# Optimization experiments

Hardware: AMD Instinct MI355X
Metric: run time of the kernel (lower is better)

## Reference

```python
import jax, jax.numpy as jnp
import numpy as np

# Similarity layer (simnets-tf), L2 similarity, ksize=3x3, stride 1, SAME padding,
# no normalization term, out_of_bounds_value = 0.
# sim[b,n,i,j] = -sum_{c,p,q} |w[n,c,p,q]| * (x_patch[b,c,i+p,j+q] - t[n,c,p,q])^2
# Expanded: -conv(x^2, |w|) + 2*conv(x, |w|*t) - sum(|w|*t^2)  (exact since pad value is 0).

B, C, H, W = 16, 64, 112, 112
N, KH, KW = 256, 3, 3
PAD = 1  # SAME padding for ksize 3


def _conv(inp, ker):
    # inp: [B,C,H',W'] padded, ker: [N,C,KH,KW] -> [B,N,H,W], VALID
    return jax.lax.conv_general_dilated(
        inp, ker, window_strides=(1, 1), padding='VALID',
        dimension_numbers=('NCHW', 'OIHW', 'NCHW'))


def setup_inputs() -> dict:
    key = jax.random.key(0)
    k1, k2, k3 = jax.random.split(key, 3)
    x = jax.random.normal(k1, (B, C, H, W), dtype=jnp.float32)
    sweights = jax.random.normal(k2, (N, C, KH, KW), dtype=jnp.float32)
    templates = jax.random.normal(k3, (N, C, KH, KW), dtype=jnp.float32)
    return {'x': x, 'sweights': sweights, 'templates': templates}


def reference(x, sweights, templates):
    w = jnp.abs(sweights)                      # layer applies tf.abs to weights
    xp = jnp.pad(x, ((0, 0), (0, 0), (PAD, PAD), (PAD, PAD)),
                 constant_values=0.0)          # out_of_bounds_value = 0
    sq_term = _conv(xp * xp, w)                # sum w * x^2 -> [B,N,H,W]
    cross = _conv(xp, w * templates)           # sum w * t * x
    const = jnp.sum(w * templates * templates, axis=(1, 2, 3))  # [N]
    return -sq_term + 2.0 * cross - const[None, :, None, None]
```

## Files before the change

### kernel.cpp

```cpp
#include <hip/hip_runtime.h>
#include <stdint.h>

#define B_ 16
#define C_ 64
#define H_ 112
#define W_ 112
#define N_ 256

typedef __attribute__((ext_vector_type(8))) short short8;
typedef __attribute__((ext_vector_type(4))) float floatx4;

typedef __attribute__((address_space(1))) const uint32_t gas_u32;
typedef __attribute__((address_space(3))) uint32_t las_u32;

__device__ __forceinline__ uint32_t f2bf_bits(float f) {
  uint32_t u = __float_as_uint(f);
  return (u + 0x7fffu + ((u >> 16) & 1u)) >> 16;
}

__global__ __launch_bounds__(256) void xform_x(const float* __restrict__ x,
                                               uint32_t* __restrict__ xq) {
  __shared__ float ls[64][113];
  int bi = blockIdx.x;
  int b = bi / H_, i = bi % H_;
  const float* xbase = x + ((size_t)b * C_) * (H_ * W_) + (size_t)i * W_;
  for (int idx = threadIdx.x; idx < C_ * W_; idx += 256) {
    int c = idx / W_, j = idx - c * W_;
    ls[c][j] = xbase[(size_t)c * (H_ * W_) + j];
  }
  __syncthreads();
  uint32_t* orow = xq + ((size_t)(b * H_ + i)) * (W_ * C_);
  for (int idx = threadIdx.x; idx < W_ * C_; idx += 256) {
    int j = idx >> 6, c = idx & 63;
    float v = ls[c][j];
    float v2 = v * v;
    orow[idx] = f2bf_bits(v) | (f2bf_bits(v2) << 16);
  }
}

__global__ __launch_bounds__(64) void prep_wc(const float* __restrict__ sw,
                                              const float* __restrict__ tp,
                                              uint32_t* __restrict__ Wg,
                                              float* __restrict__ cN) {
  int n = blockIdx.x, c = threadIdx.x;
  int cg = c >> 5, ci = c & 31;
  int kk = ci >> 4, pos = ci & 15;
  const float* swp = sw + (size_t)(n * C_ + c) * 9;
  const float* tpp = tp + (size_t)(n * C_ + c) * 9;
  float s = 0.f;
#pragma unroll
  for (int tap = 0; tap < 9; ++tap) {
    float w = fabsf(swp[tap]);
    float t = tpp[tap];
    s += w * t * t;
    uint32_t v = f2bf_bits(2.0f * w * t) | (f2bf_bits(-w) << 16);
    Wg[(size_t)(((cg * 9 + tap) * 2 + kk) * (N_ * 16)) + n * 16 + pos] = v;
  }
#pragma unroll
  for (int off = 32; off > 0; off >>= 1) s += __shfl_down(s, off);
  if (c == 0) cN[n] = s;
}

__global__ __launch_bounds__(512, 4) void sim_main(const uint32_t* __restrict__ xq,
                                                   const uint32_t* __restrict__ Wg,
                                                   const float* __restrict__ cN,
                                                   float* __restrict__ out) {
  __shared__ uint32_t xs[18 * 18 * 32];
  __shared__ uint32_t ws[2 * 2048];

  int bx = blockIdx.x;
  int nb = bx & 1;
  bx >>= 1;
  int b = bx / 49;
  int rem = bx - b * 49;
  int rt = rem / 7, ct = rem - rt * 7;
  int r0 = rt * 16, c0 = ct * 16;
  int tid = threadIdx.x;
  int lane = tid & 63, wv = tid >> 6;
  int wn = wv & 1, wp = wv >> 1;
  int l15 = lane & 15, l4 = lane >> 4;

  floatx4 acc[4][4];
#pragma unroll
  for (int a = 0; a < 4; ++a)
#pragma unroll
    for (int p = 0; p < 4; ++p) acc[a][p] = (floatx4){0.f, 0.f, 0.f, 0.f};

  const uint32_t* xim = xq + (size_t)b * (H_ * W_ * C_);
  const uint32_t* wslice = Wg + nb * 2048;

  auto stage_xs = [&](int cg) {
    for (int idx = tid; idx < 324 * 8; idx += 512) {
      int s = idx >> 3, ch = idx & 7;
      int row = s / 18, col = s - row * 18;
      int gi = r0 - 1 + row, gj = c0 - 1 + col;
      uint4 v = make_uint4(0u, 0u, 0u, 0u);
      if ((unsigned)gi < (unsigned)H_ && (unsigned)gj < (unsigned)W_)
        v = *(const uint4*)(xim + ((size_t)(gi * W_ + gj)) * C_ + cg * 32 + ch * 4);
      *(uint4*)(&xs[s * 32 + ((ch ^ (s & 7)) << 2)]) = v;
    }
  };
  auto stage_w = [&](int step) {
    const uint32_t* g = wslice + (size_t)step * (N_ * 16) + wv * 256 + lane * 4;
    uint32_t* l = &ws[(step & 1) * 2048 + wv * 256];
    __builtin_amdgcn_global_load_lds((gas_u32*)g, (las_u32*)l, 16, 0, 0);
  };

  stage_xs(0);
  stage_w(0);
  __syncthreads();

  int awb = (wn * 64 + l15) * 16 + l4 * 4;

#pragma unroll 1
  for (int s = 0; s < 36; ++s) {
    if (s < 35) stage_w(s + 1);
    if (s == 18) {
      stage_xs(1);
      __syncthreads();
    }
    int t2 = (s < 18) ? s : s - 18;
    int tap = t2 >> 1, kk = t2 & 1;
    int dp = tap / 3, dq = tap - dp * 3;
    int chb = kk * 4 + l4;
    int buf = s & 1;

    short8 af[4], bfr[4];
#pragma unroll
    for (int nt = 0; nt < 4; ++nt)
      af[nt] = *(const short8*)(&ws[buf * 2048 + awb + nt * 256]);
#pragma unroll
    for (int pt = 0; pt < 4; ++pt) {
      int st = (wp * 4 + pt + dp) * 18 + l15 + dq;
      bfr[pt] = *(const short8*)(&xs[st * 32 + ((chb ^ (st & 7)) << 2)]);
    }
#pragma unroll
    for (int nt = 0; nt < 4; ++nt)
#pragma unroll
      for (int pt = 0; pt < 4; ++pt)
        acc[nt][pt] =
            __builtin_amdgcn_mfma_f32_16x16x32_bf16(af[nt], bfr[pt], acc[nt][pt], 0, 0, 0);
    if (s < 35) __syncthreads();
  }

#pragma unroll
  for (int nt = 0; nt < 4; ++nt) {
#pragma unroll
    for (int v = 0; v < 4; ++v) {
      int n = nb * 128 + wn * 64 + nt * 16 + l4 * 4 + v;
      float cv = cN[n];
#pragma unroll
      for (int pt = 0; pt < 4; ++pt) {
        int r = r0 + wp * 4 + pt;
        int col = c0 + l15;
        out[(((size_t)b * N_ + n) * H_ + r) * W_ + col] = acc[nt][pt][v] - cv;
      }
    }
  }
}

extern "C" void kernel_launch(void* const* d_in, const int* in_sizes, int n_in,
                              void* d_out, int out_size, void* d_ws, size_t ws_size,
                              hipStream_t stream) {
  const float* x = (const float*)d_in[0];
  const float* sw = (const float*)d_in[1];
  const float* tp = (const float*)d_in[2];
  float* out = (float*)d_out;

  const size_t xq_bytes = (size_t)B_ * H_ * W_ * C_ * 4;
  const size_t wg_bytes = (size_t)2 * 9 * 2 * N_ * 16 * 4;
  uint32_t* xq = (uint32_t*)d_ws;
  uint32_t* Wg = (uint32_t*)((char*)d_ws + xq_bytes);
  float* cN = (float*)((char*)d_ws + xq_bytes + wg_bytes);

  xform_x<<<dim3(B_ * H_), dim3(256), 0, stream>>>(x, xq);
  prep_wc<<<dim3(N_), dim3(64), 0, stream>>>(sw, tp, Wg, cN);
  sim_main<<<dim3(2 * B_ * 7 * 7), dim3(512), 0, stream>>>(xq, Wg, cN, out);
}
```

Before: 380.9 us.

## Deepen weight prefetch to four buffers and restage input in 16-channel chunks

Weight tiles are now prefetched two steps ahead into a four-slot LDS ring. The full __syncthreads per step is replaced with an explicit vmcnt wait followed by s_barrier, so one global->LDS load can stay in flight. The input tile is staged in four 16-channel chunks using a padded row stride of 20 words instead of the XOR swizzle, and the weight global layout is reordered to match the new fragment addressing. The aim is to hide weight-load latency behind MFMA work, at the cost of more frequent input restaging and its extra barriers.

```diff
diff --git a/kernel.cpp b/kernel.cpp
--- a/kernel.cpp
+++ b/kernel.cpp
@@ -43,10 +43,10 @@
                                               uint32_t* __restrict__ Wg,
                                               float* __restrict__ cN) {
   int n = blockIdx.x, c = threadIdx.x;
-  int cg = c >> 5, ci = c & 31;
-  int kk = ci >> 4, pos = ci & 15;
+  int cgq = c >> 4, pos = c & 15;
   const float* swp = sw + (size_t)(n * C_ + c) * 9;
   const float* tpp = tp + (size_t)(n * C_ + c) * 9;
+  int dw = ((n >> 4) << 8) + ((pos >> 2) << 6) + ((n & 15) << 2) + (pos & 3);
   float s = 0.f;
 #pragma unroll
   for (int tap = 0; tap < 9; ++tap) {
@@ -54,7 +54,7 @@
     float t = tpp[tap];
     s += w * t * t;
     uint32_t v = f2bf_bits(2.0f * w * t) | (f2bf_bits(-w) << 16);
-    Wg[(size_t)(((cg * 9 + tap) * 2 + kk) * (N_ * 16)) + n * 16 + pos] = v;
+    Wg[(size_t)(cgq * 9 + tap) * (N_ * 16) + dw] = v;
   }
 #pragma unroll
   for (int off = 32; off > 0; off >>= 1) s += __shfl_down(s, off);
@@ -65,8 +65,8 @@
                                                    const uint32_t* __restrict__ Wg,
                                                    const float* __restrict__ cN,
                                                    float* __restrict__ out) {
-  __shared__ uint32_t xs[18 * 18 * 32];
-  __shared__ uint32_t ws[2 * 2048];
+  __shared__ uint32_t xs[324 * 20];
+  __shared__ uint32_t ws[4 * 2048];
 
   int bx = blockIdx.x;
   int nb = bx & 1;
@@ -87,43 +87,42 @@
     for (int p = 0; p < 4; ++p) acc[a][p] = (floatx4){0.f, 0.f, 0.f, 0.f};
 
   const uint32_t* xim = xq + (size_t)b * (H_ * W_ * C_);
-  const uint32_t* wslice = Wg + nb * 2048;
+  const uint32_t* wbase = Wg + nb * 2048;
 
-  auto stage_xs = [&](int cg) {
-    for (int idx = tid; idx < 324 * 8; idx += 512) {
-      int s = idx >> 3, ch = idx & 7;
+  auto stage_xs = [&](int cgq) {
+    for (int idx = tid; idx < 324 * 4; idx += 512) {
+      int s = idx >> 2, ch = idx & 3;
       int row = s / 18, col = s - row * 18;
       int gi = r0 - 1 + row, gj = c0 - 1 + col;
       uint4 v = make_uint4(0u, 0u, 0u, 0u);
       if ((unsigned)gi < (unsigned)H_ && (unsigned)gj < (unsigned)W_)
-        v = *(const uint4*)(xim + ((size_t)(gi * W_ + gj)) * C_ + cg * 32 + ch * 4);
-      *(uint4*)(&xs[s * 32 + ((ch ^ (s & 7)) << 2)]) = v;
+        v = *(const uint4*)(xim + ((size_t)(gi * W_ + gj)) * C_ + cgq * 16 + ch * 4);
+      *(uint4*)(&xs[s * 20 + ch * 4]) = v;
     }
   };
-  auto stage_w = [&](int step) {
-    const uint32_t* g = wslice + (size_t)step * (N_ * 16) + wv * 256 + lane * 4;
-    uint32_t* l = &ws[(step & 1) * 2048 + wv * 256];
+  auto stage_w = [&](int s) {
+    const uint32_t* g = wbase + (size_t)s * 4096 + wv * 256 + lane * 4;
+    uint32_t* l = &ws[(s & 3) * 2048 + wv * 256];
     __builtin_amdgcn_global_load_lds((gas_u32*)g, (las_u32*)l, 16, 0, 0);
   };
 
   stage_xs(0);
   stage_w(0);
+  stage_w(1);
   __syncthreads();
 
-  int awb = (wn * 64 + l15) * 16 + l4 * 4;
+  int awb = wn * 1024 + l4 * 64 + l15 * 4;
 
 #pragma unroll 1
   for (int s = 0; s < 36; ++s) {
-    if (s < 35) stage_w(s + 1);
-    if (s == 18) {
-      stage_xs(1);
+    if (s && s % 9 == 0) {
+      stage_xs(s / 9);
       __syncthreads();
     }
-    int t2 = (s < 18) ? s : s - 18;
-    int tap = t2 >> 1, kk = t2 & 1;
+    if (s < 34) stage_w(s + 2);
+    int tap = s % 9;
     int dp = tap / 3, dq = tap - dp * 3;
-    int chb = kk * 4 + l4;
-    int buf = s & 1;
+    int buf = s & 3;
 
     short8 af[4], bfr[4];
 #pragma unroll
@@ -132,7 +131,7 @@
 #pragma unroll
     for (int pt = 0; pt < 4; ++pt) {
       int st = (wp * 4 + pt + dp) * 18 + l15 + dq;
-      bfr[pt] = *(const short8*)(&xs[st * 32 + ((chb ^ (st & 7)) << 2)]);
+      bfr[pt] = *(const short8*)(&xs[st * 20 + l4 * 4]);
     }
 #pragma unroll
     for (int nt = 0; nt < 4; ++nt)
@@ -140,7 +139,15 @@
       for (int pt = 0; pt < 4; ++pt)
         acc[nt][pt] =
             __builtin_amdgcn_mfma_f32_16x16x32_bf16(af[nt], bfr[pt], acc[nt][pt], 0, 0, 0);
-    if (s < 35) __syncthreads();
+
+    if (s < 35) {
+      if (s < 34)
+        asm volatile("s_waitcnt vmcnt(1)" ::: "memory");
+      else
+        asm volatile("s_waitcnt vmcnt(0)" ::: "memory");
+      __builtin_amdgcn_s_barrier();
+      asm volatile("" ::: "memory");
+    }
   }
 
 #pragma unroll
@@ -168,7 +175,7 @@
   float* out = (float*)d_out;
 
   const size_t xq_bytes = (size_t)B_ * H_ * W_ * C_ * 4;
-  const size_t wg_bytes = (size_t)2 * 9 * 2 * N_ * 16 * 4;
+  const size_t wg_bytes = (size_t)36 * N_ * 16 * 4;
   uint32_t* xq = (uint32_t*)d_ws;
   uint32_t* Wg = (uint32_t*)((char*)d_ws + xq_bytes);
   float* cN = (float*)((char*)d_ws + xq_bytes + wg_bytes);
```

New measurement: 390.3 us. 2.5% more time.

## Cover all 256 filters per block, swizzle weight layout, vectorize input transform

Applied to the files above, without the earlier changes.

The main kernel now computes all 256 output filters per block instead of splitting them across two blocks. This halves the grid and stops each input tile from being staged twice, and it doubles the per-wave accumulators, which lowers occupancy (launch bounds 4 to 2, dynamic LDS). The weight buffer is laid out in an XOR-swizzled order so LDS fragment reads avoid bank conflicts. MFMA sections are raised in priority with setprio. The x transform kernel now uses float4 loads and uint4 stores.

```diff
diff --git a/kernel.cpp b/kernel.cpp
--- a/kernel.cpp
+++ b/kernel.cpp
@@ -24,17 +24,25 @@
   int bi = blockIdx.x;
   int b = bi / H_, i = bi % H_;
   const float* xbase = x + ((size_t)b * C_) * (H_ * W_) + (size_t)i * W_;
-  for (int idx = threadIdx.x; idx < C_ * W_; idx += 256) {
-    int c = idx / W_, j = idx - c * W_;
-    ls[c][j] = xbase[(size_t)c * (H_ * W_) + j];
+  for (int idx = threadIdx.x; idx < C_ * 28; idx += 256) {
+    int c = idx / 28, j4 = (idx - c * 28) * 4;
+    float4 v = *(const float4*)(xbase + (size_t)c * (H_ * W_) + j4);
+    ls[c][j4] = v.x;
+    ls[c][j4 + 1] = v.y;
+    ls[c][j4 + 2] = v.z;
+    ls[c][j4 + 3] = v.w;
   }
   __syncthreads();
   uint32_t* orow = xq + ((size_t)(b * H_ + i)) * (W_ * C_);
-  for (int idx = threadIdx.x; idx < W_ * C_; idx += 256) {
-    int j = idx >> 6, c = idx & 63;
-    float v = ls[c][j];
-    float v2 = v * v;
-    orow[idx] = f2bf_bits(v) | (f2bf_bits(v2) << 16);
+  for (int idx = threadIdx.x; idx < W_ * 16; idx += 256) {
+    int j = idx >> 4, c4 = (idx & 15) * 4;
+    float a0 = ls[c4][j], a1 = ls[c4 + 1][j], a2 = ls[c4 + 2][j], a3 = ls[c4 + 3][j];
+    uint4 o;
+    o.x = f2bf_bits(a0) | (f2bf_bits(a0 * a0) << 16);
+    o.y = f2bf_bits(a1) | (f2bf_bits(a1 * a1) << 16);
+    o.z = f2bf_bits(a2) | (f2bf_bits(a2 * a2) << 16);
+    o.w = f2bf_bits(a3) | (f2bf_bits(a3 * a3) << 16);
+    *(uint4*)(orow + j * 64 + c4) = o;
   }
 }
 
@@ -43,10 +51,12 @@
                                               uint32_t* __restrict__ Wg,
                                               float* __restrict__ cN) {
   int n = blockIdx.x, c = threadIdx.x;
-  int cg = c >> 5, ci = c & 31;
-  int kk = ci >> 4, pos = ci & 15;
+  int cg = c >> 5, kk = (c >> 4) & 1, ci = c & 15;
   const float* swp = sw + (size_t)(n * C_ + c) * 9;
   const float* tpp = tp + (size_t)(n * C_ + c) * 9;
+  int sn = n >> 1;
+  int cpos = ((n & 1) << 2) | (ci >> 2);
+  int phys = sn * 32 + ((cpos ^ (sn & 7)) << 2) + (ci & 3);
   float s = 0.f;
 #pragma unroll
   for (int tap = 0; tap < 9; ++tap) {
@@ -54,23 +64,22 @@
     float t = tpp[tap];
     s += w * t * t;
     uint32_t v = f2bf_bits(2.0f * w * t) | (f2bf_bits(-w) << 16);
-    Wg[(size_t)(((cg * 9 + tap) * 2 + kk) * (N_ * 16)) + n * 16 + pos] = v;
+    Wg[(size_t)(cg * 18 + tap * 2 + kk) * 4096 + phys] = v;
   }
 #pragma unroll
   for (int off = 32; off > 0; off >>= 1) s += __shfl_down(s, off);
   if (c == 0) cN[n] = s;
 }
 
-__global__ __launch_bounds__(512, 4) void sim_main(const uint32_t* __restrict__ xq,
+__global__ __launch_bounds__(512, 2) void sim_main(const uint32_t* __restrict__ xq,
                                                    const uint32_t* __restrict__ Wg,
                                                    const float* __restrict__ cN,
                                                    float* __restrict__ out) {
-  __shared__ uint32_t xs[18 * 18 * 32];
-  __shared__ uint32_t ws[2 * 2048];
+  extern __shared__ uint32_t smem[];
+  uint32_t* xs = smem;
+  uint32_t* ws = smem + 10368;
 
   int bx = blockIdx.x;
-  int nb = bx & 1;
-  bx >>= 1;
   int b = bx / 49;
   int rem = bx - b * 49;
   int rt = rem / 7, ct = rem - rt * 7;
@@ -80,14 +89,21 @@
   int wn = wv & 1, wp = wv >> 1;
   int l15 = lane & 15, l4 = lane >> 4;
 
-  floatx4 acc[4][4];
-#pragma unroll
-  for (int a = 0; a < 4; ++a)
+  floatx4 acc[8][4];
+#pragma unroll
+  for (int a = 0; a < 8; ++a)
 #pragma unroll
     for (int p = 0; p < 4; ++p) acc[a][p] = (floatx4){0.f, 0.f, 0.f, 0.f};
 
   const uint32_t* xim = xq + (size_t)b * (H_ * W_ * C_);
-  const uint32_t* wslice = Wg + nb * 2048;
+
+  int afoff[8];
+#pragma unroll
+  for (int nt = 0; nt < 8; ++nt) {
+    int n = wn * 128 + nt * 16 + l15;
+    int sn = n >> 1;
+    afoff[nt] = sn * 32 + (((((n & 1) << 2) | l4) ^ (sn & 7)) << 2);
+  }
 
   auto stage_xs = [&](int cg) {
     for (int idx = tid; idx < 324 * 8; idx += 512) {
@@ -100,54 +116,58 @@
       *(uint4*)(&xs[s * 32 + ((ch ^ (s & 7)) << 2)]) = v;
     }
   };
-  auto stage_w = [&](int step) {
-    const uint32_t* g = wslice + (size_t)step * (N_ * 16) + wv * 256 + lane * 4;
-    uint32_t* l = &ws[(step & 1) * 2048 + wv * 256];
-    __builtin_amdgcn_global_load_lds((gas_u32*)g, (las_u32*)l, 16, 0, 0);
+  auto stage_w = [&](int s) {
+#pragma unroll
+    for (int k = 0; k < 2; ++k) {
+      const uint32_t* g = Wg + (size_t)s * 4096 + k * 2048 + wv * 256 + lane * 4;
+      uint32_t* l = &ws[(s & 1) * 4096 + k * 2048 + wv * 256];
+      __builtin_amdgcn_global_load_lds((gas_u32*)g, (las_u32*)l, 16, 0, 0);
+    }
   };
 
   stage_xs(0);
   stage_w(0);
   __syncthreads();
 
-  int awb = (wn * 64 + l15) * 16 + l4 * 4;
-
 #pragma unroll 1
   for (int s = 0; s < 36; ++s) {
-    if (s < 35) stage_w(s + 1);
     if (s == 18) {
       stage_xs(1);
       __syncthreads();
+      stage_w(19);
+    } else if (s < 35) {
+      stage_w(s + 1);
     }
     int t2 = (s < 18) ? s : s - 18;
-    int tap = t2 >> 1, kk = t2 & 1;
+    int tap = t2 >> 1, kk = s & 1;
     int dp = tap / 3, dq = tap - dp * 3;
+    const uint32_t* wsb = ws + (s & 1) * 4096;
     int chb = kk * 4 + l4;
-    int buf = s & 1;
-
-    short8 af[4], bfr[4];
-#pragma unroll
-    for (int nt = 0; nt < 4; ++nt)
-      af[nt] = *(const short8*)(&ws[buf * 2048 + awb + nt * 256]);
+
+    short8 bfr[4];
 #pragma unroll
     for (int pt = 0; pt < 4; ++pt) {
       int st = (wp * 4 + pt + dp) * 18 + l15 + dq;
       bfr[pt] = *(const short8*)(&xs[st * 32 + ((chb ^ (st & 7)) << 2)]);
     }
-#pragma unroll
-    for (int nt = 0; nt < 4; ++nt)
+    __builtin_amdgcn_s_setprio(1);
+#pragma unroll
+    for (int nt = 0; nt < 8; ++nt) {
+      short8 af = *(const short8*)(wsb + afoff[nt]);
 #pragma unroll
       for (int pt = 0; pt < 4; ++pt)
         acc[nt][pt] =
-            __builtin_amdgcn_mfma_f32_16x16x32_bf16(af[nt], bfr[pt], acc[nt][pt], 0, 0, 0);
+            __builtin_amdgcn_mfma_f32_16x16x32_bf16(af, bfr[pt], acc[nt][pt], 0, 0, 0);
+    }
+    __builtin_amdgcn_s_setprio(0);
     if (s < 35) __syncthreads();
   }
 
 #pragma unroll
-  for (int nt = 0; nt < 4; ++nt) {
+  for (int nt = 0; nt < 8; ++nt) {
 #pragma unroll
     for (int v = 0; v < 4; ++v) {
-      int n = nb * 128 + wn * 64 + nt * 16 + l4 * 4 + v;
+      int n = wn * 128 + nt * 16 + l4 * 4 + v;
       float cv = cN[n];
 #pragma unroll
       for (int pt = 0; pt < 4; ++pt) {
@@ -168,12 +188,20 @@
   float* out = (float*)d_out;
 
   const size_t xq_bytes = (size_t)B_ * H_ * W_ * C_ * 4;
-  const size_t wg_bytes = (size_t)2 * 9 * 2 * N_ * 16 * 4;
+  const size_t wg_bytes = (size_t)36 * 4096 * 4;
   uint32_t* xq = (uint32_t*)d_ws;
   uint32_t* Wg = (uint32_t*)((char*)d_ws + xq_bytes);
   float* cN = (float*)((char*)d_ws + xq_bytes + wg_bytes);
 
+  const int smem_bytes = (10368 + 2 * 4096) * 4;
+  static int smem_set = 0;
+  if (!smem_set) {
+    hipFuncSetAttribute((const void*)sim_main,
+                        hipFuncAttributeMaxDynamicSharedMemorySize, smem_bytes);
+    smem_set = 1;
+  }
+
   xform_x<<<dim3(B_ * H_), dim3(256), 0, stream>>>(x, xq);
   prep_wc<<<dim3(N_), dim3(64), 0, stream>>>(sw, tp, Wg, cN);
-  sim_main<<<dim3(2 * B_ * 7 * 7), dim3(512), 0, stream>>>(xq, Wg, cN, out);
-}
+  sim_main<<<dim3(B_ * 7 * 7), dim3(512), smem_bytes, stream>>>(xq, Wg, cN, out);
+}
```

Result: slower. 409.1 us (+7.4%).
